# Kernel optimization log

Measured on AMD Instinct MI355X. Metric: run time of the kernel, lower is better.

Reference implementation:

```python
import jax, jax.numpy as jnp
import numpy as np

V, N, D = 3, 131072, 512
NEG_SLOPE = 0.01  # torch F.leaky_relu default


def setup_inputs() -> dict:
    key = jax.random.key(0)
    k1, k2, k3 = jax.random.split(key, 3)
    xs = jax.random.normal(k1, (V, N, D), dtype=jnp.float32)
    # Linear(n_hidden, 1): weight [1, D] -> stored as [D], bias [1]
    alpha_w = jax.random.normal(k2, (D,), dtype=jnp.float32) * (1.0 / np.sqrt(D))
    alpha_b = jax.random.normal(k3, (1,), dtype=jnp.float32) * 0.01
    return {"xs": xs, "alpha_w": alpha_w, "alpha_b": alpha_b}


def reference(xs, alpha_w, alpha_b):
    # per-view attention logit: leaky_relu(x @ w + b) -> [V, N]
    logits = jax.nn.leaky_relu(jnp.einsum('vnd,d->vn', xs, alpha_w) + alpha_b[0],
                               negative_slope=NEG_SLOPE)
    # softmax across views (torch cat dim=1 then softmax dim=1)
    attn = jax.nn.softmax(logits, axis=0)  # [V, N]
    # dropout is identity in eval mode (reference baseline)
    # sparse_diag(attn[:, i]) @ x_i is just a broadcasted row-scale; sum views
    return jnp.einsum('vn,vnd->nd', attn, xs)  # [N, D]
```

## Files before the change

### kernel.cpp

```cpp
#include <hip/hip_runtime.h>

#define NVIEWS 3
#define NROWS 131072
#define DDIM 512
#define NEG_SLOPE 0.01f

typedef float v4f __attribute__((ext_vector_type(4)));

__global__ __launch_bounds__(256) void adaptive_fusion_kernel(
    const float* __restrict__ xs,
    const float* __restrict__ alpha_w,
    const float* __restrict__ alpha_b,
    float* __restrict__ out)
{
    const int lane = threadIdx.x & 63;
    const int wib  = threadIdx.x >> 6;
    const int wpb  = blockDim.x >> 6;
    const int gw   = blockIdx.x * wpb + wib;
    const int nw   = gridDim.x * wpb;

    const v4f* w4 = (const v4f*)alpha_w;
    const v4f w0 = w4[lane];
    const v4f w1 = w4[64 + lane];
    const float bias = alpha_b[0];

    for (int n = gw; n < NROWS; n += nw) {
        v4f x[NVIEWS][2];
        float dot[NVIEWS];
#pragma unroll
        for (int v = 0; v < NVIEWS; ++v) {
            const v4f* xr = (const v4f*)(xs + ((size_t)v * NROWS + n) * DDIM);
            x[v][0] = xr[lane];
            x[v][1] = xr[64 + lane];
            v4f p = x[v][0] * w0 + x[v][1] * w1;
            dot[v] = p[0] + p[1] + p[2] + p[3];
        }

#pragma unroll
        for (int off = 32; off; off >>= 1) {
#pragma unroll
            for (int v = 0; v < NVIEWS; ++v)
                dot[v] += __shfl_xor(dot[v], off, 64);
        }

        float l[NVIEWS];
#pragma unroll
        for (int v = 0; v < NVIEWS; ++v) {
            const float t = dot[v] + bias;
            l[v] = t > 0.0f ? t : NEG_SLOPE * t;
        }

        const float m = fmaxf(fmaxf(l[0], l[1]), l[2]);
        float e[NVIEWS];
        float s = 0.0f;
#pragma unroll
        for (int v = 0; v < NVIEWS; ++v) { e[v] = __expf(l[v] - m); s += e[v]; }
        const float inv = 1.0f / s;
        const float a0 = e[0] * inv, a1 = e[1] * inv, a2 = e[2] * inv;

        const v4f o0 = a0 * x[0][0] + a1 * x[1][0] + a2 * x[2][0];
        const v4f o1 = a0 * x[0][1] + a1 * x[1][1] + a2 * x[2][1];
        v4f* orow = (v4f*)(out + (size_t)n * DDIM);
        orow[lane]      = o0;
        orow[64 + lane] = o1;
    }
}

extern "C" void kernel_launch(void* const* d_in, const int* in_sizes, int n_in,
                              void* d_out, int out_size, void* d_ws, size_t ws_size,
                              hipStream_t stream) {
    const float* xs      = (const float*)d_in[0];
    const float* alpha_w = (const float*)d_in[1];
    const float* alpha_b = (const float*)d_in[2];
    float* out = (float*)d_out;

    dim3 grid(2048), block(256);
    hipLaunchKernelGGL(adaptive_fusion_kernel, grid, block, 0, stream,
                       xs, alpha_w, alpha_b, out);
}
```

Baseline: 1.087 ms.

## Assign contiguous row chunks per wave with two-row batching and nontemporal accesses

Each wave now processes a fixed contiguous block of rows, two rows per iteration, instead of a grid-strided loop. Loads for both rows across all three views are issued before any reduction, which raises the number of memory requests in flight per wave. Loads and stores use nontemporal builtins to avoid cache pollution on streaming data. This costs more registers per thread and hardcodes the problem size into the partitioning.

```diff
diff --git a/kernel.cpp b/kernel.cpp
--- a/kernel.cpp
+++ b/kernel.cpp
@@ -5,7 +5,21 @@
 #define DDIM 512
 #define NEG_SLOPE 0.01f
 
+#define NBLOCKS 2048
+#define WAVES_PER_BLOCK 4
+#define NWAVES (NBLOCKS * WAVES_PER_BLOCK)
+#define ROWS_PER_WAVE (NROWS / NWAVES)
+#define ROWS_PER_ITER 2
+#define NITER (ROWS_PER_WAVE / ROWS_PER_ITER)
+
 typedef float v4f __attribute__((ext_vector_type(4)));
+
+__device__ __forceinline__ v4f ntload4(const v4f* p) {
+    return __builtin_nontemporal_load(p);
+}
+__device__ __forceinline__ void ntstore4(v4f* p, v4f v) {
+    __builtin_nontemporal_store(v, p);
+}
 
 __global__ __launch_bounds__(256) void adaptive_fusion_kernel(
     const float* __restrict__ xs,
@@ -14,55 +28,77 @@
     float* __restrict__ out)
 {
     const int lane = threadIdx.x & 63;
-    const int wib  = threadIdx.x >> 6;
-    const int wpb  = blockDim.x >> 6;
-    const int gw   = blockIdx.x * wpb + wib;
-    const int nw   = gridDim.x * wpb;
+    const int wave = (blockIdx.x * blockDim.x + threadIdx.x) >> 6;
 
     const v4f* w4 = (const v4f*)alpha_w;
     const v4f w0 = w4[lane];
     const v4f w1 = w4[64 + lane];
     const float bias = alpha_b[0];
 
-    for (int n = gw; n < NROWS; n += nw) {
-        v4f x[NVIEWS][2];
-        float dot[NVIEWS];
+    const size_t row0 = (size_t)wave * ROWS_PER_WAVE;
+    const float* p0 = xs + row0 * DDIM;
+    const float* p1 = p0 + (size_t)NROWS * DDIM;
+    const float* p2 = p1 + (size_t)NROWS * DDIM;
+    float* po = out + row0 * DDIM;
+
+#pragma unroll 1
+    for (int it = 0; it < NITER; ++it) {
+        v4f x[ROWS_PER_ITER][NVIEWS][2];
+
 #pragma unroll
-        for (int v = 0; v < NVIEWS; ++v) {
-            const v4f* xr = (const v4f*)(xs + ((size_t)v * NROWS + n) * DDIM);
-            x[v][0] = xr[lane];
-            x[v][1] = xr[64 + lane];
-            v4f p = x[v][0] * w0 + x[v][1] * w1;
-            dot[v] = p[0] + p[1] + p[2] + p[3];
+        for (int r = 0; r < ROWS_PER_ITER; ++r) {
+            const v4f* b0 = (const v4f*)(p0 + r * DDIM);
+            const v4f* b1 = (const v4f*)(p1 + r * DDIM);
+            const v4f* b2 = (const v4f*)(p2 + r * DDIM);
+            x[r][0][0] = ntload4(b0 + lane);
+            x[r][0][1] = ntload4(b0 + 64 + lane);
+            x[r][1][0] = ntload4(b1 + lane);
+            x[r][1][1] = ntload4(b1 + 64 + lane);
+            x[r][2][0] = ntload4(b2 + lane);
+            x[r][2][1] = ntload4(b2 + 64 + lane);
+        }
+
+        float d[ROWS_PER_ITER * NVIEWS];
+#pragma unroll
+        for (int r = 0; r < ROWS_PER_ITER; ++r) {
+#pragma unroll
+            for (int v = 0; v < NVIEWS; ++v) {
+                v4f p = x[r][v][0] * w0 + x[r][v][1] * w1;
+                d[r * NVIEWS + v] = p[0] + p[1] + p[2] + p[3];
+            }
         }
 
 #pragma unroll
         for (int off = 32; off; off >>= 1) {
 #pragma unroll
-            for (int v = 0; v < NVIEWS; ++v)
-                dot[v] += __shfl_xor(dot[v], off, 64);
+            for (int i = 0; i < ROWS_PER_ITER * NVIEWS; ++i)
+                d[i] += __shfl_xor(d[i], off, 64);
         }
 
-        float l[NVIEWS];
 #pragma unroll
-        for (int v = 0; v < NVIEWS; ++v) {
-            const float t = dot[v] + bias;
-            l[v] = t > 0.0f ? t : NEG_SLOPE * t;
+        for (int r = 0; r < ROWS_PER_ITER; ++r) {
+            float l[NVIEWS];
+#pragma unroll
+            for (int v = 0; v < NVIEWS; ++v) {
+                const float t = d[r * NVIEWS + v] + bias;
+                l[v] = t > 0.0f ? t : NEG_SLOPE * t;
+            }
+            const float m = fmaxf(fmaxf(l[0], l[1]), l[2]);
+            float e0 = __expf(l[0] - m), e1 = __expf(l[1] - m), e2 = __expf(l[2] - m);
+            const float inv = 1.0f / (e0 + e1 + e2);
+            const float a0 = e0 * inv, a1 = e1 * inv, a2 = e2 * inv;
+
+            const v4f o0 = a0 * x[r][0][0] + a1 * x[r][1][0] + a2 * x[r][2][0];
+            const v4f o1 = a0 * x[r][0][1] + a1 * x[r][1][1] + a2 * x[r][2][1];
+            v4f* orow = (v4f*)(po + r * DDIM);
+            ntstore4(orow + lane, o0);
+            ntstore4(orow + 64 + lane, o1);
         }
 
-        const float m = fmaxf(fmaxf(l[0], l[1]), l[2]);
-        float e[NVIEWS];
-        float s = 0.0f;
-#pragma unroll
-        for (int v = 0; v < NVIEWS; ++v) { e[v] = __expf(l[v] - m); s += e[v]; }
-        const float inv = 1.0f / s;
-        const float a0 = e[0] * inv, a1 = e[1] * inv, a2 = e[2] * inv;
-
-        const v4f o0 = a0 * x[0][0] + a1 * x[1][0] + a2 * x[2][0];
-        const v4f o1 = a0 * x[0][1] + a1 * x[1][1] + a2 * x[2][1];
-        v4f* orow = (v4f*)(out + (size_t)n * DDIM);
-        orow[lane]      = o0;
-        orow[64 + lane] = o1;
+        p0 += ROWS_PER_ITER * DDIM;
+        p1 += ROWS_PER_ITER * DDIM;
+        p2 += ROWS_PER_ITER * DDIM;
+        po += ROWS_PER_ITER * DDIM;
     }
 }
 
@@ -74,7 +110,7 @@
     const float* alpha_b = (const float*)d_in[2];
     float* out = (float*)d_out;
 
-    dim3 grid(2048), block(256);
+    dim3 grid(NBLOCKS), block(WAVES_PER_BLOCK * 64);
     hipLaunchKernelGGL(adaptive_fusion_kernel, grid, block, 0, stream,
                        xs, alpha_w, alpha_b, out);
 }
```

Result: no change. 1.069 ms (-1.7%).
